# Performance work log

Measured on AMD Instinct MI355X. Metric: run time of the kernel, lower is better.

Reference implementation:

```python
import jax, jax.numpy as jnp
from jax import lax
import numpy as np

B, H, W = 16, 512, 512
NBINS = 256
MARGIN_EYE = 12
BLUR_SIZE = 5
ALPHA_SKIN, ALPHA_EYE, ALPHA_LIP = 0.3, 0.8, 0.1


def de_norm(x):
    return jnp.clip((x + 1.0) * 0.5, 0.0, 1.0)


def renorm(x):
    return x * 2.0 - 1.0


def _match_channel(src, ref, w_s, w_r):
    # src/ref: (P,) pixel values in [0,255]; w_s/w_r: (P,) mask weights
    b_s = jnp.clip(src.astype(jnp.int32), 0, NBINS - 1)
    b_r = jnp.clip(ref.astype(jnp.int32), 0, NBINS - 1)
    h_s = jnp.zeros((NBINS,), src.dtype).at[b_s].add(w_s)   # masked histogram
    h_r = jnp.zeros((NBINS,), ref.dtype).at[b_r].add(w_r)
    cdf_s = jnp.cumsum(h_s) / jnp.maximum(jnp.sum(h_s), 1e-6)
    cdf_r = jnp.cumsum(h_r) / jnp.maximum(jnp.sum(h_r), 1e-6)
    # CDF-matching transfer table (equiv. of cal_trans in PSGAN/EleGANt)
    table = jnp.clip(jnp.searchsorted(cdf_r, cdf_s), 0, NBINS - 1).astype(src.dtype)
    return table[b_s]


def masked_his_match(image_s, image_r, mask_s, mask_r):
    # image: (3,H,W), mask: (1,H,W)
    s = de_norm(image_s) * 255.0 * mask_s
    r = de_norm(image_r) * 255.0 * mask_r
    w_s = mask_s.reshape(-1)
    w_r = mask_r.reshape(-1)
    matched = jax.vmap(_match_channel, in_axes=(0, 0, None, None))(
        s.reshape(3, -1), r.reshape(3, -1), w_s, w_r).reshape(s.shape)
    matched = jnp.where(mask_s > 0, matched, s)  # only masked pixels replaced
    return renorm(matched / 255.0)


def expand_area(mask, margin):
    # morphological dilation (max pool) of (1,H,W) mask
    k = 2 * margin + 1
    return lax.reduce_window(mask, 0.0, lax.max, (1, k, k), (1, 1, 1), 'SAME')


def mask_blur(mask, blur_size):
    # box blur; 'valid' mode: blurred support kept inside original mask
    k = blur_size
    s = lax.reduce_window(mask, 0.0, lax.add, (1, k, k), (1, 1, 1), 'SAME') / float(k * k)
    return s * mask


def generate_pgt(image_s, image_r, mask_s, mask_r, lms_s, lms_r):
    pgt = image_s
    # skin (channel 1)
    m = mask_s[1:2]
    pgt = (1.0 - m) * pgt + m * masked_his_match(image_s, image_r, m, mask_r[1:2])
    # neck (channel 4)
    m = mask_s[4:5]
    pgt = (1.0 - m) * pgt + m * masked_his_match(image_s, image_r, m, mask_r[4:5])
    # lip (channel 0)
    m = mask_s[0:1]
    pgt = (1.0 - m) * pgt + m * masked_his_match(image_s, image_r, m, mask_r[0:1])
    # eyes (channels 2,3), dilated and intersected with skin
    m_se = expand_area(jnp.sum(mask_s[2:4], axis=0, keepdims=True), MARGIN_EYE) * mask_s[1:2]
    m_re = expand_area(jnp.sum(mask_r[2:4], axis=0, keepdims=True), MARGIN_EYE) * mask_r[1:2]
    eye_match = masked_his_match(image_s, image_r, m_se, m_re)
    mb = mask_blur(m_se, BLUR_SIZE)
    pgt = (1.0 - mb) * pgt + mb * eye_match
    # fine_align (reconstructed, simplified: per-region alpha blend of reference,
    # landmark warp omitted -- helper source not provided)
    for m, a in ((mask_s[1:2], ALPHA_SKIN), (m_se, ALPHA_EYE), (mask_s[0:1], ALPHA_LIP)):
        pgt = (1.0 - a * m) * pgt + (a * m) * image_r
    return pgt


def setup_inputs() -> dict:
    key = jax.random.key(0)
    ks = jax.random.split(key, 6)
    sources = jax.random.uniform(ks[0], (B, 3, H, W), jnp.float32, -1.0, 1.0)
    targets = jax.random.uniform(ks[1], (B, 3, H, W), jnp.float32, -1.0, 1.0)
    mask_srcs = (jax.random.uniform(ks[2], (B, 5, H, W)) < 0.3).astype(jnp.float32)
    mask_tars = (jax.random.uniform(ks[3], (B, 5, H, W)) < 0.3).astype(jnp.float32)
    lms_srcs = jax.random.uniform(ks[4], (B, 68, 2), jnp.float32, 0.0, float(H))
    lms_tars = jax.random.uniform(ks[5], (B, 68, 2), jnp.float32, 0.0, float(H))
    return {"sources": sources, "targets": targets, "mask_srcs": mask_srcs,
            "mask_tars": mask_tars, "lms_srcs": lms_srcs, "lms_tars": lms_tars}


def reference(sources, targets, mask_srcs, mask_tars, lms_srcs, lms_tars):
    # vmap over batch replaces the per-sample Python loop of ComposePGT.forward
    return jax.vmap(generate_pgt)(sources, targets, mask_srcs, mask_tars, lms_srcs, lms_tars)
```

## Files before the change

### kernel.cpp

```cpp
#include <hip/hip_runtime.h>
#include <stdint.h>

#define BB 16
#define HH 512
#define WW 512
#define HW (HH*WW)
#define NB 256

#define YC 36
#define SROWS 64
#define MROWS 40
#define NYCH 15


__device__ __forceinline__ float denorm255(float x) {
    return fminf(fmaxf((x + 1.0f) * 0.5f, 0.0f), 1.0f) * 255.0f;
}
__device__ __forceinline__ float renorm_lut(int t) {
    return ((float)t / 255.0f) * 2.0f - 1.0f;
}
__device__ __forceinline__ uint32_t alignb(uint32_t hi, uint32_t lo, int r) {
    return (uint32_t)(((((uint64_t)hi) << 32) | lo) >> (8 * r));
}

__global__ void __launch_bounds__(256) fused_mask_kernel(
    const float* __restrict__ ms, const float* __restrict__ mr,
    uint32_t* __restrict__ C, uint32_t* __restrict__ mbs)
{
    __shared__ uint32_t sHor[SROWS][128];
    __shared__ uint32_t sMse[MROWS][129];

    int blk  = (blockIdx.x & 7) * 60 + (blockIdx.x >> 3);
    int ych  = blk % NYCH;
    int sb   = blk / NYCH;
    int side = sb >> 4;
    int b    = sb & 15;
    int y0   = ych * YC;

    const float* base = (side ? mr : ms) + (size_t)b * 5 * HW;
    int r0 = threadIdx.x >> 5;
    int c  = threadIdx.x & 31;

    for (int it = 0; it < 8; ++it) {
        int L  = r0 + 8 * it;
        int gy = y0 - 14 + L;
        bool inimg = (gy >= 0 && gy < HH);
        bool m1row = inimg && (L >= 12 && L < 52);
        bool owned = inimg && (L >= 14 && L < 50);

        float4 v[5][4];
        #pragma unroll
        for (int p = 0; p < 5; p++)
            #pragma unroll
            for (int j = 0; j < 4; j++) v[p][j] = make_float4(0.f, 0.f, 0.f, 0.f);

        const float* rowp = base + (size_t)gy * WW + 16 * c;
        if (inimg) {
            const float4* p2 = (const float4*)(rowp + 2 * (size_t)HW);
            const float4* p3 = (const float4*)(rowp + 3 * (size_t)HW);
            #pragma unroll
            for (int j = 0; j < 4; j++) { v[2][j] = p2[j]; v[3][j] = p3[j]; }
            if (m1row) {
                const float4* p1 = (const float4*)(rowp + (size_t)HW);
                #pragma unroll
                for (int j = 0; j < 4; j++) v[1][j] = p1[j];
            }
            if (owned) {
                const float4* p0 = (const float4*)(rowp);
                const float4* p4 = (const float4*)(rowp + 4 * (size_t)HW);
                #pragma unroll
                for (int j = 0; j < 4; j++) { v[0][j] = p0[j]; v[4][j] = p4[j]; }
            }
        }

        uint32_t Wd[4], E[4];
        #pragma unroll
        for (int j = 0; j < 4; j++) {
            uint32_t wc = 0;
            #pragma unroll
            for (int k = 0; k < 4; k++) {
                float a0 = (&v[0][j].x)[k];
                float a1 = (&v[1][j].x)[k];
                float a2 = (&v[2][j].x)[k];
                float a3 = (&v[3][j].x)[k];
                float a4 = (&v[4][j].x)[k];
                uint32_t e  = (uint32_t)(a2 + a3);
                uint32_t pb = (a0 > 0.f ? 4u : 0u) | (a1 > 0.f ? 8u : 0u)
                            | (a4 > 0.f ? 16u : 0u);
                wc |= (e | pb) << (8 * k);
            }
            Wd[j] = wc;
            E[j]  = wc & 0x03030303u;
        }

        uint32_t Lw[3], Rw[3];
        #pragma unroll
        for (int i = 0; i < 3; i++) {
            uint32_t lv = __shfl_up(E[i + 1], 1, 32);
            Lw[i] = (c == 0) ? 0u : lv;
            uint32_t rv = __shfl_down(E[i], 1, 32);
            Rw[i] = (c == 31) ? 0u : rv;
        }
        uint32_t arr[10] = {Lw[0], Lw[1], Lw[2], E[0], E[1], E[2], E[3],
                            Rw[0], Rw[1], Rw[2]};
        #pragma unroll
        for (int k = 0; k < 4; k++) {
            const int b3 = 3 + k;
            uint32_t a = arr[b3];
            #pragma unroll
            for (int s = 1; s <= 12; s++) {
                int ai = s >> 2, rrs = s & 3;
                uint32_t vp, vm;
                if (rrs == 0) {
                    vp = arr[b3 + ai];
                    vm = arr[b3 - ai];
                } else {
                    vp = alignb(arr[b3 + ai + 1], arr[b3 + ai], rrs);
                    int am = (s + 3) >> 2;
                    vm = alignb(arr[b3 - am + 1], arr[b3 - am], 4 - rrs);
                }
                a |= vp | vm;
            }
            sHor[L][4 * c + k] = Wd[k] | (a << 5);
        }
    }
    __syncthreads();

    {
        int w  = threadIdx.x & 127;
        int mg = threadIdx.x >> 7;
        for (int k = 0; k < 20; ++k) {
            int m = mg * 20 + k;
            uint32_t o = 0;
            #pragma unroll
            for (int dy = 0; dy < 25; ++dy) o |= sHor[m + dy][w];
            uint32_t vv = (o >> 5) & 0x03030303u;
            uint32_t t3 = vv & (vv >> 1) & 0x01010101u;
            vv -= t3;
            uint32_t m1 = (sHor[m + 12][w] >> 3) & 0x01010101u;
            vv &= m1 * 3u;
            sMse[m][w] = vv;
        }
    }
    __syncthreads();

    {
        int ck = threadIdx.x & 31;
        int rr = threadIdx.x >> 5;
        size_t plane = (size_t)(side * BB + b);
        uint32_t* Cp = C + plane * (HW / 4);
        uint32_t* Mp = mbs + (size_t)b * (HW / 4);
        for (int o = rr; o < YC; o += 8) {
            int gy = y0 + o;
            if (gy >= HH) break;
            uint4 cw;
            #pragma unroll
            for (int q = 0; q < 4; q++) {
                uint32_t b5 = sHor[14 + o][4 * ck + q] & 0x1F1F1F1Fu;
                uint32_t mv = sMse[o + 2][4 * ck + q];
                (&cw.x)[q] = b5 | (mv << 5);
            }
            *((uint4*)(Cp + (size_t)gy * 128 + 4 * ck)) = cw;

            if (side == 0) {
                uint32_t s[6] = {0u, 0u, 0u, 0u, 0u, 0u};
                #pragma unroll
                for (int dy = 0; dy < 5; dy++) {
                    const uint32_t* rp = sMse[o + dy];
                    if (ck > 0)  s[0] += rp[4 * ck - 1];
                    s[1] += rp[4 * ck + 0];
                    s[2] += rp[4 * ck + 1];
                    s[3] += rp[4 * ck + 2];
                    s[4] += rp[4 * ck + 3];
                    if (ck < 31) s[5] += rp[4 * ck + 4];
                }
                uint4 ob;
                #pragma unroll
                for (int k = 0; k < 4; k++) {
                    uint32_t vv = s[k + 1];
                    vv += alignb(s[k + 1], s[k],     2);
                    vv += alignb(s[k + 1], s[k],     3);
                    vv += alignb(s[k + 2], s[k + 1], 1);
                    vv += alignb(s[k + 2], s[k + 1], 2);
                    (&ob.x)[k] = vv;
                }
                *((uint4*)(Mp + (size_t)gy * 128 + 4 * ck)) = ob;
            }
        }
    }
}

#define HB 32
__device__ __forceinline__ void hist4(int* h, uint32_t cw,
                                      float4 v0, float4 v1, float4 v2)
{
    float d0[4] = {denorm255(v0.x), denorm255(v0.y), denorm255(v0.z), denorm255(v0.w)};
    float d1[4] = {denorm255(v1.x), denorm255(v1.y), denorm255(v1.z), denorm255(v1.w)};
    float d2[4] = {denorm255(v2.x), denorm255(v2.y), denorm255(v2.z), denorm255(v2.w)};
    #pragma unroll
    for (int j = 0; j < 4; j++) {
        uint32_t pb = (cw >> (8 * j)) & 0xFFu;
        if (pb & 8u) {
            atomicAdd(&h[0 * NB + min((int)d0[j], 255)], 1);
            atomicAdd(&h[1 * NB + min((int)d1[j], 255)], 1);
            atomicAdd(&h[2 * NB + min((int)d2[j], 255)], 1);
        }
        if (pb & 16u) {
            atomicAdd(&h[3 * NB + min((int)d0[j], 255)], 1);
            atomicAdd(&h[4 * NB + min((int)d1[j], 255)], 1);
            atomicAdd(&h[5 * NB + min((int)d2[j], 255)], 1);
        }
        if (pb & 4u) {
            atomicAdd(&h[6 * NB + min((int)d0[j], 255)], 1);
            atomicAdd(&h[7 * NB + min((int)d1[j], 255)], 1);
            atomicAdd(&h[8 * NB + min((int)d2[j], 255)], 1);
        }
        int mei = (int)((pb >> 5) & 3u);
        if (mei) {
            float fm = (float)mei;
            atomicAdd(&h[ 9 * NB + min((int)(d0[j] * fm), 255)], mei);
            atomicAdd(&h[10 * NB + min((int)(d1[j] * fm), 255)], mei);
            atomicAdd(&h[11 * NB + min((int)(d2[j] * fm), 255)], mei);
        }
    }
}

__global__ void __launch_bounds__(256) hist_kernel(
    const float* __restrict__ src, const float* __restrict__ tgt,
    const uint32_t* __restrict__ C, int* __restrict__ hist)
{
    int bs  = blockIdx.x / HB;
    int blk = blockIdx.x % HB;
    int b = bs >> 1, side = bs & 1;
    const float* img = (side ? tgt : src) + (size_t)b * 3 * HW;
    const float4* i0 = (const float4*)(img);
    const float4* i1 = (const float4*)(img + HW);
    const float4* i2 = (const float4*)(img + 2 * (size_t)HW);
    const uint2* pc = (const uint2*)(C + (size_t)(side * BB + b) * (HW / 4));

    __shared__ int h[2][12 * NB];
    int* hw = h[threadIdx.x >> 7];
    for (int i = threadIdx.x; i < 2 * 12 * NB; i += 256) ((int*)h)[i] = 0;
    __syncthreads();

    for (int c = blk * 256 + threadIdx.x; c < HW / 8; c += HB * 256) {
        uint2 cw = pc[c];
        float4 a0 = i0[2 * c], b0 = i0[2 * c + 1];
        float4 a1 = i1[2 * c], b1 = i1[2 * c + 1];
        float4 a2 = i2[2 * c], b2 = i2[2 * c + 1];
        hist4(hw, cw.x, a0, a1, a2);
        hist4(hw, cw.y, b0, b1, b2);
    }
    __syncthreads();
    int* gh = hist + (size_t)bs * 12 * NB;
    for (int i = threadIdx.x; i < 12 * NB; i += 256) {
        int s = h[0][i] + h[1][i];
        if (s) atomicAdd(&gh[i], s);
    }
}

__global__ void __launch_bounds__(NB) table_kernel(
    const int* __restrict__ hist, uint8_t* __restrict__ table)
{
    int idx = blockIdx.x;
    int c = idx % 3; int rest = idx / 3; int rg = rest & 3; int b = rest >> 2;
    const int* hs = hist + ((size_t)((b * 2 + 0) * 4 + rg) * 3 + c) * NB;
    const int* hr = hist + ((size_t)((b * 2 + 1) * 4 + rg) * 3 + c) * NB;
    __shared__ int a[NB];
    __shared__ float cr[NB];
    int t = threadIdx.x;

    a[t] = hs[t];
    __syncthreads();
    for (int off = 1; off < NB; off <<= 1) {
        int v = (t >= off) ? a[t - off] : 0;
        __syncthreads();
        a[t] += v;
        __syncthreads();
    }
    int totS = a[NB - 1];
    int cumS = a[t];
    __syncthreads();

    a[t] = hr[t];
    __syncthreads();
    for (int off = 1; off < NB; off <<= 1) {
        int v = (t >= off) ? a[t - off] : 0;
        __syncthreads();
        a[t] += v;
        __syncthreads();
    }
    int totR = a[NB - 1];
    cr[t] = (float)a[t] / fmaxf((float)totR, 1e-6f);
    float v = (float)cumS / fmaxf((float)totS, 1e-6f);
    __syncthreads();

    int cnt = 0;
    for (int j = 0; j < NB; j++) cnt += (cr[j] < v) ? 1 : 0;
    table[(size_t)idx * NB + t] = (uint8_t)min(cnt, 255);
}

__device__ __forceinline__ void proc4(uint32_t cw, uint32_t qw,
    float4 x0, float4 x1, float4 x2, float4 r0, float4 r1, float4 r2,
    const uint8_t* tb, float4& o0, float4& o1, float4& o2)
{
    float X0[4] = {x0.x, x0.y, x0.z, x0.w};
    float X1[4] = {x1.x, x1.y, x1.z, x1.w};
    float X2[4] = {x2.x, x2.y, x2.z, x2.w};
    float R0[4] = {r0.x, r0.y, r0.z, r0.w};
    float R1[4] = {r1.x, r1.y, r1.z, r1.w};
    float R2[4] = {r2.x, r2.y, r2.z, r2.w};
    #pragma unroll
    for (int j = 0; j < 4; j++) {
        uint32_t pb = (cw >> (8 * j)) & 0xFFu;
        float q = (float)((qw >> (8 * j)) & 0xFFu);
        float m0f = (float)((pb >> 2) & 1u);
        float m1f = (float)((pb >> 3) & 1u);
        float m4f = (float)((pb >> 4) & 1u);
        float fm  = (float)((pb >> 5) & 3u);
        float d0 = denorm255(X0[j]), d1 = denorm255(X1[j]), d2 = denorm255(X2[j]);
        float p0 = X0[j], p1 = X1[j], p2 = X2[j];
        {
            float e0 = renorm_lut(tb[0 * NB + min((int)(d0 * m1f), 255)]);
            float e1 = renorm_lut(tb[1 * NB + min((int)(d1 * m1f), 255)]);
            float e2 = renorm_lut(tb[2 * NB + min((int)(d2 * m1f), 255)]);
            p0 = (1.0f - m1f) * p0 + m1f * e0;
            p1 = (1.0f - m1f) * p1 + m1f * e1;
            p2 = (1.0f - m1f) * p2 + m1f * e2;
        }
        {
            float e0 = renorm_lut(tb[3 * NB + min((int)(d0 * m4f), 255)]);
            float e1 = renorm_lut(tb[4 * NB + min((int)(d1 * m4f), 255)]);
            float e2 = renorm_lut(tb[5 * NB + min((int)(d2 * m4f), 255)]);
            p0 = (1.0f - m4f) * p0 + m4f * e0;
            p1 = (1.0f - m4f) * p1 + m4f * e1;
            p2 = (1.0f - m4f) * p2 + m4f * e2;
        }
        {
            float e0 = renorm_lut(tb[6 * NB + min((int)(d0 * m0f), 255)]);
            float e1 = renorm_lut(tb[7 * NB + min((int)(d1 * m0f), 255)]);
            float e2 = renorm_lut(tb[8 * NB + min((int)(d2 * m0f), 255)]);
            p0 = (1.0f - m0f) * p0 + m0f * e0;
            p1 = (1.0f - m0f) * p1 + m0f * e1;
            p2 = (1.0f - m0f) * p2 + m0f * e2;
        }
        {
            float mb = (q * (1.0f / 25.0f)) * fm;
            float e0 = renorm_lut(tb[ 9 * NB + min((int)(d0 * fm), 255)]);
            float e1 = renorm_lut(tb[10 * NB + min((int)(d1 * fm), 255)]);
            float e2 = renorm_lut(tb[11 * NB + min((int)(d2 * fm), 255)]);
            p0 = (1.0f - mb) * p0 + mb * e0;
            p1 = (1.0f - mb) * p1 + mb * e1;
            p2 = (1.0f - mb) * p2 + mb * e2;
        }
        float a = 0.3f * m1f;
        p0 = (1.0f - a) * p0 + a * R0[j];
        p1 = (1.0f - a) * p1 + a * R1[j];
        p2 = (1.0f - a) * p2 + a * R2[j];
        a = 0.8f * fm;
        p0 = (1.0f - a) * p0 + a * R0[j];
        p1 = (1.0f - a) * p1 + a * R1[j];
        p2 = (1.0f - a) * p2 + a * R2[j];
        a = 0.1f * m0f;
        p0 = (1.0f - a) * p0 + a * R0[j];
        p1 = (1.0f - a) * p1 + a * R1[j];
        p2 = (1.0f - a) * p2 + a * R2[j];
        (&o0.x)[j] = p0; (&o1.x)[j] = p1; (&o2.x)[j] = p2;
    }
}

__global__ void __launch_bounds__(256) compose_kernel(
    const float* __restrict__ src, const float* __restrict__ tgt,
    const uint32_t* __restrict__ C, const uint32_t* __restrict__ mbs,
    const uint8_t* __restrict__ table, float* __restrict__ out)
{
    int t = blockIdx.x * 256 + threadIdx.x;
    int b = t >> 15;
    int c = t & 32767;

    __shared__ uint8_t tb[12 * NB];
    {
        const uint32_t* gt = (const uint32_t*)(table + (size_t)b * 12 * NB);
        uint32_t* tw = (uint32_t*)tb;
        for (int i = threadIdx.x; i < 12 * NB / 4; i += 256) tw[i] = gt[i];
    }
    __syncthreads();

    const float4* s0 = (const float4*)(src + (size_t)b * 3 * HW);
    const float4* s1 = s0 + HW / 4;
    const float4* s2 = s1 + HW / 4;
    const float4* t0 = (const float4*)(tgt + (size_t)b * 3 * HW);
    const float4* t1 = t0 + HW / 4;
    const float4* t2 = t1 + HW / 4;
    const uint2* pc = (const uint2*)(C + (size_t)b * (HW / 4));
    const uint2* qc = (const uint2*)(mbs + (size_t)b * (HW / 4));
    float4* o0 = (float4*)(out + (size_t)b * 3 * HW);
    float4* o1 = o0 + HW / 4;
    float4* o2 = o1 + HW / 4;

    uint2 cw = pc[c];
    uint2 qw = qc[c];
    float4 xa0 = s0[2 * c], xb0 = s0[2 * c + 1];
    float4 xa1 = s1[2 * c], xb1 = s1[2 * c + 1];
    float4 xa2 = s2[2 * c], xb2 = s2[2 * c + 1];
    float4 ra0 = t0[2 * c], rb0 = t0[2 * c + 1];
    float4 ra1 = t1[2 * c], rb1 = t1[2 * c + 1];
    float4 ra2 = t2[2 * c], rb2 = t2[2 * c + 1];

    float4 oa0, oa1, oa2, ob0, ob1, ob2;
    proc4(cw.x, qw.x, xa0, xa1, xa2, ra0, ra1, ra2, tb, oa0, oa1, oa2);
    proc4(cw.y, qw.y, xb0, xb1, xb2, rb0, rb1, rb2, tb, ob0, ob1, ob2);

    o0[2 * c] = oa0; o0[2 * c + 1] = ob0;
    o1[2 * c] = oa1; o1[2 * c + 1] = ob1;
    o2[2 * c] = oa2; o2[2 * c + 1] = ob2;
}

extern "C" void kernel_launch(void* const* d_in, const int* in_sizes, int n_in,
                              void* d_out, int out_size, void* d_ws, size_t ws_size,
                              hipStream_t stream) {
    const float* src = (const float*)d_in[0];
    const float* tgt = (const float*)d_in[1];
    const float* ms  = (const float*)d_in[2];
    const float* mr  = (const float*)d_in[3];
    float* out = (float*)d_out;

    uint8_t* ws = (uint8_t*)d_ws;
    uint32_t* C   = (uint32_t*)(ws);
    uint32_t* mbs = (uint32_t*)(ws + (size_t)4 * BB * HW);
    int* hist     = (int*)(ws + (size_t)5 * BB * HW);
    uint8_t* table = ws + (size_t)5 * BB * HW + (size_t)2 * BB * 12 * NB * 4;

    hipMemsetAsync(hist, 0, (size_t)2 * BB * 12 * NB * sizeof(int), stream);

    fused_mask_kernel<<<2 * BB * NYCH, 256, 0, stream>>>(ms, mr, C, mbs);
    hist_kernel<<<2 * BB * HB, 256, 0, stream>>>(src, tgt, C, hist);
    table_kernel<<<BB * 4 * 3, NB, 0, stream>>>(hist, table);
    compose_kernel<<<BB * (HW / 8) / 256, 256, 0, stream>>>(src, tgt, C, mbs, table, out);
}
```

Measured before the change: 335.1 us.

## Fuse histogram accumulation into mask kernel using shared-memory mask codes

Removes the separate hist_kernel and accumulates the per-sample masked histograms at the end of fused_mask_kernel. The per-pixel class codes are rebuilt from the sHor and sMse shared tiles instead of being read back from global C, and one kernel launch is dropped. In exchange, each block's shared memory grows by 24KB for two histogram copies, which may lower occupancy. The histogram work now runs over only 480 blocks instead of 1024, so there is less parallelism for the atomic-heavy phase.

```diff
diff --git a/kernel.cpp b/kernel.cpp
--- a/kernel.cpp
+++ b/kernel.cpp
@@ -23,12 +23,49 @@
     return (uint32_t)(((((uint64_t)hi) << 32) | lo) >> (8 * r));
 }
 
+__device__ __forceinline__ void hist4(int* h, uint32_t cw,
+                                      float4 v0, float4 v1, float4 v2)
+{
+    float d0[4] = {denorm255(v0.x), denorm255(v0.y), denorm255(v0.z), denorm255(v0.w)};
+    float d1[4] = {denorm255(v1.x), denorm255(v1.y), denorm255(v1.z), denorm255(v1.w)};
+    float d2[4] = {denorm255(v2.x), denorm255(v2.y), denorm255(v2.z), denorm255(v2.w)};
+    #pragma unroll
+    for (int j = 0; j < 4; j++) {
+        uint32_t pb = (cw >> (8 * j)) & 0xFFu;
+        if (pb & 8u) {
+            atomicAdd(&h[0 * NB + min((int)d0[j], 255)], 1);
+            atomicAdd(&h[1 * NB + min((int)d1[j], 255)], 1);
+            atomicAdd(&h[2 * NB + min((int)d2[j], 255)], 1);
+        }
+        if (pb & 16u) {
+            atomicAdd(&h[3 * NB + min((int)d0[j], 255)], 1);
+            atomicAdd(&h[4 * NB + min((int)d1[j], 255)], 1);
+            atomicAdd(&h[5 * NB + min((int)d2[j], 255)], 1);
+        }
+        if (pb & 4u) {
+            atomicAdd(&h[6 * NB + min((int)d0[j], 255)], 1);
+            atomicAdd(&h[7 * NB + min((int)d1[j], 255)], 1);
+            atomicAdd(&h[8 * NB + min((int)d2[j], 255)], 1);
+        }
+        int mei = (int)((pb >> 5) & 3u);
+        if (mei) {
+            float fm = (float)mei;
+            atomicAdd(&h[ 9 * NB + min((int)(d0[j] * fm), 255)], mei);
+            atomicAdd(&h[10 * NB + min((int)(d1[j] * fm), 255)], mei);
+            atomicAdd(&h[11 * NB + min((int)(d2[j] * fm), 255)], mei);
+        }
+    }
+}
+
 __global__ void __launch_bounds__(256) fused_mask_kernel(
     const float* __restrict__ ms, const float* __restrict__ mr,
-    uint32_t* __restrict__ C, uint32_t* __restrict__ mbs)
+    const float* __restrict__ src, const float* __restrict__ tgt,
+    uint32_t* __restrict__ C, uint32_t* __restrict__ mbs,
+    int* __restrict__ hist)
 {
     __shared__ uint32_t sHor[SROWS][128];
     __shared__ uint32_t sMse[MROWS][129];
+    __shared__ int h[2][12 * NB];
 
     int blk  = (blockIdx.x & 7) * 60 + (blockIdx.x >> 3);
     int ych  = blk % NYCH;
@@ -41,6 +78,8 @@
     int r0 = threadIdx.x >> 5;
     int c  = threadIdx.x & 31;
 
+    for (int i = threadIdx.x; i < 2 * 12 * NB; i += 256) ((int*)h)[i] = 0;
+
     for (int it = 0; it < 8; ++it) {
         int L  = r0 + 8 * it;
         int gy = y0 - 14 + L;
@@ -54,8 +93,8 @@
             #pragma unroll
             for (int j = 0; j < 4; j++) v[p][j] = make_float4(0.f, 0.f, 0.f, 0.f);
 
-        const float* rowp = base + (size_t)gy * WW + 16 * c;
         if (inimg) {
+            const float* rowp = base + (size_t)gy * WW + 16 * c;
             const float4* p2 = (const float4*)(rowp + 2 * (size_t)HW);
             const float4* p3 = (const float4*)(rowp + 3 * (size_t)HW);
             #pragma unroll
@@ -188,74 +227,36 @@
             }
         }
     }
-}
-
-#define HB 32
-__device__ __forceinline__ void hist4(int* h, uint32_t cw,
-                                      float4 v0, float4 v1, float4 v2)
-{
-    float d0[4] = {denorm255(v0.x), denorm255(v0.y), denorm255(v0.z), denorm255(v0.w)};
-    float d1[4] = {denorm255(v1.x), denorm255(v1.y), denorm255(v1.z), denorm255(v1.w)};
-    float d2[4] = {denorm255(v2.x), denorm255(v2.y), denorm255(v2.z), denorm255(v2.w)};
-    #pragma unroll
-    for (int j = 0; j < 4; j++) {
-        uint32_t pb = (cw >> (8 * j)) & 0xFFu;
-        if (pb & 8u) {
-            atomicAdd(&h[0 * NB + min((int)d0[j], 255)], 1);
-            atomicAdd(&h[1 * NB + min((int)d1[j], 255)], 1);
-            atomicAdd(&h[2 * NB + min((int)d2[j], 255)], 1);
-        }
-        if (pb & 16u) {
-            atomicAdd(&h[3 * NB + min((int)d0[j], 255)], 1);
-            atomicAdd(&h[4 * NB + min((int)d1[j], 255)], 1);
-            atomicAdd(&h[5 * NB + min((int)d2[j], 255)], 1);
-        }
-        if (pb & 4u) {
-            atomicAdd(&h[6 * NB + min((int)d0[j], 255)], 1);
-            atomicAdd(&h[7 * NB + min((int)d1[j], 255)], 1);
-            atomicAdd(&h[8 * NB + min((int)d2[j], 255)], 1);
-        }
-        int mei = (int)((pb >> 5) & 3u);
-        if (mei) {
-            float fm = (float)mei;
-            atomicAdd(&h[ 9 * NB + min((int)(d0[j] * fm), 255)], mei);
-            atomicAdd(&h[10 * NB + min((int)(d1[j] * fm), 255)], mei);
-            atomicAdd(&h[11 * NB + min((int)(d2[j] * fm), 255)], mei);
-        }
-    }
-}
-
-__global__ void __launch_bounds__(256) hist_kernel(
-    const float* __restrict__ src, const float* __restrict__ tgt,
-    const uint32_t* __restrict__ C, int* __restrict__ hist)
-{
-    int bs  = blockIdx.x / HB;
-    int blk = blockIdx.x % HB;
-    int b = bs >> 1, side = bs & 1;
-    const float* img = (side ? tgt : src) + (size_t)b * 3 * HW;
-    const float4* i0 = (const float4*)(img);
-    const float4* i1 = (const float4*)(img + HW);
-    const float4* i2 = (const float4*)(img + 2 * (size_t)HW);
-    const uint2* pc = (const uint2*)(C + (size_t)(side * BB + b) * (HW / 4));
-
-    __shared__ int h[2][12 * NB];
-    int* hw = h[threadIdx.x >> 7];
-    for (int i = threadIdx.x; i < 2 * 12 * NB; i += 256) ((int*)h)[i] = 0;
-    __syncthreads();
-
-    for (int c = blk * 256 + threadIdx.x; c < HW / 8; c += HB * 256) {
-        uint2 cw = pc[c];
-        float4 a0 = i0[2 * c], b0 = i0[2 * c + 1];
-        float4 a1 = i1[2 * c], b1 = i1[2 * c + 1];
-        float4 a2 = i2[2 * c], b2 = i2[2 * c + 1];
-        hist4(hw, cw.x, a0, a1, a2);
-        hist4(hw, cw.y, b0, b1, b2);
-    }
-    __syncthreads();
-    int* gh = hist + (size_t)bs * 12 * NB;
-    for (int i = threadIdx.x; i < 12 * NB; i += 256) {
-        int s = h[0][i] + h[1][i];
-        if (s) atomicAdd(&gh[i], s);
+
+    {
+        int* hw = h[threadIdx.x >> 7];
+        const float* img = (side ? tgt : src) + (size_t)b * 3 * HW;
+        const float4* i0 = (const float4*)(img);
+        const float4* i1 = (const float4*)(img + HW);
+        const float4* i2 = (const float4*)(img + 2 * (size_t)HW);
+        for (int idx = threadIdx.x; idx < YC * 64; idx += 256) {
+            int o = idx >> 6, g = idx & 63;
+            int gy = y0 + o;
+            if (gy >= HH) continue;
+            int cidx = gy * 64 + g;
+            uint32_t cwx = (sHor[14 + o][2 * g]     & 0x1F1F1F1Fu)
+                         | (sMse[o + 2][2 * g]     << 5);
+            uint32_t cwy = (sHor[14 + o][2 * g + 1] & 0x1F1F1F1Fu)
+                         | (sMse[o + 2][2 * g + 1] << 5);
+            float4 a0 = i0[2 * cidx], b0v = i0[2 * cidx + 1];
+            float4 a1 = i1[2 * cidx], b1v = i1[2 * cidx + 1];
+            float4 a2 = i2[2 * cidx], b2v = i2[2 * cidx + 1];
+            hist4(hw, cwx, a0, a1, a2);
+            hist4(hw, cwy, b0v, b1v, b2v);
+        }
+    }
+    __syncthreads();
+    {
+        int* gh = hist + (size_t)(b * 2 + side) * 12 * NB;
+        for (int i = threadIdx.x; i < 12 * NB; i += 256) {
+            int s = h[0][i] + h[1][i];
+            if (s) atomicAdd(&gh[i], s);
+        }
     }
 }
 
@@ -433,8 +434,7 @@
 
     hipMemsetAsync(hist, 0, (size_t)2 * BB * 12 * NB * sizeof(int), stream);
 
-    fused_mask_kernel<<<2 * BB * NYCH, 256, 0, stream>>>(ms, mr, C, mbs);
-    hist_kernel<<<2 * BB * HB, 256, 0, stream>>>(src, tgt, C, hist);
+    fused_mask_kernel<<<2 * BB * NYCH, 256, 0, stream>>>(ms, mr, src, tgt, C, mbs, hist);
     table_kernel<<<BB * 4 * 3, NB, 0, stream>>>(hist, table);
     compose_kernel<<<BB * (HW / 8) / 256, 256, 0, stream>>>(src, tgt, C, mbs, table, out);
 }
```

Measured after the change: 327.3 us. 1.02x faster.
